# Kernel optimization log

Hardware: AMD Instinct MI355X
Metric: run time of the kernel (lower is better)

Reference implementation:

```python
import jax, jax.numpy as jnp
import numpy as np

MAX_WARPING_WINDOW = None  # matches init kwarg (None => full window, no masking)


def _pairwise_euclidean(x, y):
    # x: (B, F, Tx), y: (B, F, Ty) -> (B, Tx, Ty)
    # ||x_t - y_s||_2 computed via the expanded quadratic form (one GEMM instead
    # of materializing the (B, F, Tx, Ty) difference tensor like the torch code).
    x2 = jnp.sum(x * x, axis=1)                      # (B, Tx)
    y2 = jnp.sum(y * y, axis=1)                      # (B, Ty)
    xy = jnp.einsum('bft,bfs->bts', x, y)            # (B, Tx, Ty)
    d2 = jnp.maximum(x2[:, :, None] + y2[:, None, :] - 2.0 * xy, 0.0)
    return jnp.sqrt(d2)


def _dtw(cost):
    # cost: (B, Tx, Ty). Classic DTW DP:
    #   dtw[i, j] = cost[i-1, j-1] + min(dtw[i-1, j], dtw[i, j-1], dtw[i-1, j-1])
    # outer scan over rows i, inner scan over columns j (carries dtw[i, j-1]).
    B, Tx, Ty = cost.shape
    dt = cost.dtype
    INF = jnp.array(jnp.inf, dt)
    cost_t = jnp.transpose(cost, (1, 2, 0))          # (Tx, Ty, B)

    def row_step(carry, cost_row):
        prev_row, left = carry                       # prev_row: (Ty, B) = dtw[i-1, 1:], left: (B,) = dtw[i-1, 0]
        prev_shift = jnp.concatenate([left[None, :], prev_row[:-1]], axis=0)  # dtw[i-1, j-1]
        a = jnp.minimum(prev_row, prev_shift)        # min(dtw[i-1, j], dtw[i-1, j-1])

        def col_step(cur_left, ac):
            a_j, c_j = ac                            # each (B,)
            cur = c_j + jnp.minimum(a_j, cur_left)   # cur_left = dtw[i, j-1]
            return cur, cur

        _, cur_row = jax.lax.scan(col_step, jnp.full((B,), INF, dt), (a, cost_row))
        return (cur_row, jnp.full((B,), INF, dt)), None

    # row 0 of the DP: dtw[0, 0] = 0, dtw[0, j>0] = inf
    init = (jnp.full((Ty, B), INF, dt), jnp.zeros((B,), dt))
    (last_row, _), _ = jax.lax.scan(row_step, init, cost_t)
    return last_row[-1]                              # dtw[Tx, Ty], shape (B,)


def setup_inputs() -> dict:
    key = jax.random.key(0)
    kx, ky = jax.random.split(key)
    B, F, T = 128, 128, 512
    x = jax.random.normal(kx, (B, F, T), dtype=jnp.float32)
    y = jax.random.normal(ky, (B, F, T), dtype=jnp.float32)
    return {"x": x, "y": y}


def reference(x, y):
    cost = _pairwise_euclidean(x, y)                 # (B, Tx, Ty)
    if MAX_WARPING_WINDOW is not None:
        Tx, Ty = cost.shape[1], cost.shape[2]
        p = jnp.arange(Tx)[:, None]
        q = jnp.arange(Ty)[None, :]
        cost = jnp.where(jnp.abs(p - q) <= MAX_WARPING_WINDOW, cost, jnp.inf)
    return _dtw(cost)
```

## Files before the change

### kernel.cpp

```cpp
#include <hip/hip_runtime.h>
#include <stdint.h>

#define B_ 128
#define F_ 128
#define T_ 512
#define TS 64
#define DIAG_N 1024

#define BIGV 1e30f

typedef __attribute__((ext_vector_type(8))) short     bf16x8;
typedef __attribute__((ext_vector_type(4))) float     f32x4;
typedef __attribute__((ext_vector_type(8))) _Float16  half8;

static __device__ __forceinline__ unsigned short f32_to_bf16(float f) {
    union { float f; uint32_t u; } v; v.f = f;
    const uint32_t u = v.u + 0x7fffu + ((v.u >> 16) & 1u);
    return (unsigned short)(u >> 16);
}

static __device__ __forceinline__ float wave_shr1(float src, float fill) {
    const int r = __builtin_amdgcn_update_dpp(
        __builtin_bit_cast(int, fill), __builtin_bit_cast(int, src),
        0x138 , 0xf, 0xf, false);
    return __builtin_bit_cast(float, r);
}
static __device__ __forceinline__ float wave_shl1(float src, float fill) {
    const int r = __builtin_amdgcn_update_dpp(
        __builtin_bit_cast(int, fill), __builtin_bit_cast(int, src),
        0x130 , 0xf, 0xf, false);
    return __builtin_bit_cast(float, r);
}

__global__ __launch_bounds__(256) void dtw_prep_kernel(
    const float* __restrict__ x, const float* __restrict__ y,
    unsigned short* __restrict__ xt, unsigned short* __restrict__ yt,
    float* __restrict__ nx, float* __restrict__ ny)
{
    const int tch = blockIdx.x;
    const int b   = blockIdx.y;
    const int z   = blockIdx.z;
    const int tid = threadIdx.x;
    const int t0  = tch * 64;

    const float* src      = (z == 0 ? x : y) + (size_t)b * F_ * T_;
    unsigned short* dst   = (z == 0 ? xt : yt) + (size_t)b * T_ * F_;
    float* nd             = (z == 0 ? nx : ny) + (size_t)b * T_;

    __shared__ float S[F_][65];

    const int fr = tid >> 4;
    const int q  = (tid & 15) * 4;
#pragma unroll
    for (int p = 0; p < 8; ++p) {
        const int f = p * 16 + fr;
        const float4 v = *(const float4*)(src + (size_t)f * T_ + t0 + q);
        S[f][q] = v.x; S[f][q + 1] = v.y; S[f][q + 2] = v.z; S[f][q + 3] = v.w;
    }
    __syncthreads();

    if (tid < 64) {
        float s = 0.f;
#pragma unroll
        for (int f = 0; f < F_; ++f) { const float v = S[f][tid]; s = fmaf(v, v, s); }
        nd[t0 + tid] = s;
    }

    const int tl = tid >> 2;
    const int fb = (tid & 3) * 32;
    uint32_t pk[16];
#pragma unroll
    for (int e = 0; e < 16; ++e) {
        const uint32_t lo = f32_to_bf16(S[fb + 2 * e][tl]);
        const uint32_t hi = f32_to_bf16(S[fb + 2 * e + 1][tl]);
        pk[e] = lo | (hi << 16);
    }
    uint32_t* o = (uint32_t*)(dst + (size_t)(t0 + tl) * F_ + fb);
#pragma unroll
    for (int e = 0; e < 16; e += 4)
        *(uint4*)(o + e) = make_uint4(pk[e], pk[e + 1], pk[e + 2], pk[e + 3]);
}

__global__ __launch_bounds__(256) void dtw_cost_kernel(
    const unsigned short* __restrict__ xt, const unsigned short* __restrict__ yt,
    const float* __restrict__ nx, const float* __restrict__ ny,
    unsigned short* __restrict__ costD, int b0)
{
    const int tj  = blockIdx.x;
    const int ti  = blockIdx.y;
    const int bl  = blockIdx.z;
    const int b   = b0 + bl;
    const int tid = threadIdx.x;
    const int gi0 = ti * TS;
    const int gj0 = tj * TS;

    const int w    = tid >> 6;
    const int lane = tid & 63;
    const int l15  = lane & 15;
    const int hi   = lane >> 4;

    __shared__ __align__(16) char smem[16384];
    unsigned short* Ys = (unsigned short*)smem;

    {
        const int l16 = tid & 15;
#pragma unroll
        for (int p = 0; p < 4; ++p) {
            const int row = p * 16 + (tid >> 4);
            const uint4 vy = *(const uint4*)(yt + ((size_t)b * T_ + gj0 + row) * F_ + l16 * 8);
            const int byt = (row * 256 + l16 * 16) ^ ((row & 7) << 4);
            *(uint4*)((char*)Ys + byt) = vy;
        }
    }

    const unsigned short* xb = xt + ((size_t)b * T_ + gi0 + 16 * w + l15) * F_ + hi * 8;
    const bf16x8 A0 = *(const bf16x8*)(xb);
    const bf16x8 A1 = *(const bf16x8*)(xb + 32);
    const bf16x8 A2 = *(const bf16x8*)(xb + 64);
    const bf16x8 A3 = *(const bf16x8*)(xb + 96);

    const float4 x2r = *(const float4*)(nx + (size_t)b * T_ + gi0 + 16 * w + 4 * hi);
    float y2c[4];
#pragma unroll
    for (int nt = 0; nt < 4; ++nt)
        y2c[nt] = ny[(size_t)b * T_ + gj0 + nt * 16 + l15];
    const float x2v[4] = {x2r.x, x2r.y, x2r.z, x2r.w};

    __syncthreads();

    f32x4 acc[4] = {};
#pragma unroll
    for (int kb = 0; kb < 4; ++kb) {
        const int koff = kb * 64 + hi * 16;
        const bf16x8 a = (kb == 0) ? A0 : (kb == 1) ? A1 : (kb == 2) ? A2 : A3;
#pragma unroll
        for (int nt = 0; nt < 4; ++nt) {
            const int col = nt * 16 + l15;
            const bf16x8 bb = *(const bf16x8*)((const char*)Ys +
                               ((col * 256 + koff) ^ ((col & 7) << 4)));
            acc[nt] = __builtin_amdgcn_mfma_f32_16x16x32_bf16(a, bb, acc[nt], 0, 0, 0);
        }
    }

    __syncthreads();
    unsigned short* Ts = (unsigned short*)smem;
#pragma unroll
    for (int nt = 0; nt < 4; ++nt) {
        const int col = nt * 16 + l15;
#pragma unroll
        for (int r = 0; r < 4; ++r) {
            const int row = 16 * w + hi * 4 + r;
            const float c = sqrtf(fmaxf(x2v[r] + y2c[nt] - 2.f * acc[nt][r], 0.f));
            const _Float16 hv = (_Float16)c;
            Ts[row * 67 + col] = *(const unsigned short*)&hv;
        }
    }
    __syncthreads();

    unsigned short* outD = costD + (size_t)bl * (DIAG_N * (size_t)T_);
    const int tbase = gi0 + gj0;
#pragma unroll
    for (int q = 0; q < 16; ++q) {
        const int g = q * 4 + w;
        const int d = (lane <= g) ? g : g + 64;
        outD[(size_t)(tbase + d) * T_ + gj0 + lane] = Ts[(d - lane) * 67 + lane];
    }
}

__global__ __launch_bounds__(128, 1) void dtw_dp_bidi(
    const unsigned short* __restrict__ costD, float* __restrict__ out, int b0)
{
    const int bl  = blockIdx.x;
    const int tid = threadIdx.x;
    const int w   = tid >> 6;
    const int L   = tid & 63;
    const unsigned short* gbase = costD + (size_t)bl * (DIAG_N * (size_t)T_) + 8 * L;

    __shared__ __align__(16) unsigned short ringF[32][T_];
    __shared__ __align__(16) unsigned short ringB[32][T_];
    __shared__ __align__(16) float bb2[T_];
    __shared__ __align__(16) float bb3[T_];

    float va0 = BIGV, va1 = BIGV, va2 = BIGV, va3 = BIGV,
          va4 = BIGV, va5 = BIGV, va6 = BIGV, va7 = BIGV;
    float vb0 = BIGV, vb1 = BIGV, vb2 = BIGV, vb3 = BIGV,
          vb4 = BIGV, vb5 = BIGV, vb6 = BIGV, vb7 = BIGV;
    float s2c;
    half8 ca0, ca1, ca2, ca3, ca4, ca5, ca6, ca7;
    half8 cb0, cb1, cb2, cb3, cb4, cb5, cb6, cb7;

#define GLD(RING, row, slot)                                                \
    __builtin_amdgcn_global_load_lds(                                       \
        (const __attribute__((address_space(1))) void*)(gbase + (size_t)(row) * T_), \
        (__attribute__((address_space(3))) void*)(&RING[slot][0]), 16, 0, 0)

#define GLD8F(blk) do {                                                     \
    const int r0_ = (blk) * 8, s0_ = ((blk) & 3) * 8;                       \
    GLD(ringF, r0_ + 0, s0_ + 0); GLD(ringF, r0_ + 1, s0_ + 1);             \
    GLD(ringF, r0_ + 2, s0_ + 2); GLD(ringF, r0_ + 3, s0_ + 3);             \
    GLD(ringF, r0_ + 4, s0_ + 4); GLD(ringF, r0_ + 5, s0_ + 5);             \
    GLD(ringF, r0_ + 6, s0_ + 6); GLD(ringF, r0_ + 7, s0_ + 7);             \
} while (0)

#define GLD8B(blk) do {                                                     \
    const int v0_ = (blk) * 8, s0_ = ((blk) & 3) * 8;                       \
    GLD(ringB, 1022 - (v0_ + 0), s0_ + 0); GLD(ringB, 1022 - (v0_ + 1), s0_ + 1); \
    GLD(ringB, 1022 - (v0_ + 2), s0_ + 2); GLD(ringB, 1022 - (v0_ + 3), s0_ + 3); \
    GLD(ringB, 1022 - (v0_ + 4), s0_ + 4); GLD(ringB, 1022 - (v0_ + 5), s0_ + 5); \
    GLD(ringB, 1022 - (v0_ + 6), s0_ + 6); GLD(ringB, 1022 - (v0_ + 7), s0_ + 7); \
} while (0)

#define WAITV(n)                                                            \
    do { asm volatile("s_waitcnt vmcnt(" #n ")" ::: "memory");              \
         __builtin_amdgcn_sched_barrier(0); } while (0)

#define SB __builtin_amdgcn_sched_barrier(0)

#define RL8(RING, BK, blk) do {                                             \
    const unsigned short* rp_ = &RING[((blk) & 3) * 8][8 * L];              \
    BK##0 = *(const half8*)(rp_ + 0 * T_);                                  \
    BK##1 = *(const half8*)(rp_ + 1 * T_);                                  \
    BK##2 = *(const half8*)(rp_ + 2 * T_);                                  \
    BK##3 = *(const half8*)(rp_ + 3 * T_);                                  \
    BK##4 = *(const half8*)(rp_ + 4 * T_);                                  \
    BK##5 = *(const half8*)(rp_ + 5 * T_);                                  \
    BK##6 = *(const half8*)(rp_ + 6 * T_);                                  \
    BK##7 = *(const half8*)(rp_ + 7 * T_);                                  \
} while (0)

#define STEPF_A(hh) do {                                                    \
    const float s1 = wave_shr1(va7, BIGV);                                  \
    const float n0 = (float)hh[0] + fminf(fminf(va0, s1),  s2c);            \
    const float n1 = (float)hh[1] + fminf(fminf(va1, va0), vb0);            \
    const float n2 = (float)hh[2] + fminf(fminf(va2, va1), vb1);            \
    const float n3 = (float)hh[3] + fminf(fminf(va3, va2), vb2);            \
    const float n4 = (float)hh[4] + fminf(fminf(va4, va3), vb3);            \
    const float n5 = (float)hh[5] + fminf(fminf(va5, va4), vb4);            \
    const float n6 = (float)hh[6] + fminf(fminf(va6, va5), vb5);            \
    const float n7 = (float)hh[7] + fminf(fminf(va7, va6), vb6);            \
    s2c = s1;                                                               \
    vb0 = n0; vb1 = n1; vb2 = n2; vb3 = n3;                                 \
    vb4 = n4; vb5 = n5; vb6 = n6; vb7 = n7;                                 \
} while (0)

#define STEPF_B(hh) do {                                                    \
    const float s1 = wave_shr1(vb7, BIGV);                                  \
    const float n0 = (float)hh[0] + fminf(fminf(vb0, s1),  s2c);            \
    const float n1 = (float)hh[1] + fminf(fminf(vb1, vb0), va0);            \
    const float n2 = (float)hh[2] + fminf(fminf(vb2, vb1), va1);            \
    const float n3 = (float)hh[3] + fminf(fminf(vb3, vb2), va2);            \
    const float n4 = (float)hh[4] + fminf(fminf(vb4, vb3), va3);            \
    const float n5 = (float)hh[5] + fminf(fminf(vb5, vb4), va4);            \
    const float n6 = (float)hh[6] + fminf(fminf(vb6, vb5), va5);            \
    const float n7 = (float)hh[7] + fminf(fminf(vb7, vb6), va6);            \
    s2c = s1;                                                               \
    va0 = n0; va1 = n1; va2 = n2; va3 = n3;                                 \
    va4 = n4; va5 = n5; va6 = n6; va7 = n7;                                 \
} while (0)

#define STEPB_A(hh) do {                                                    \
    const float s1 = wave_shl1(va0, BIGV);                                  \
    const float n7 = (float)hh[7] + fminf(fminf(va7, s1),  s2c);            \
    const float n6 = (float)hh[6] + fminf(fminf(va6, va7), vb7);            \
    const float n5 = (float)hh[5] + fminf(fminf(va5, va6), vb6);            \
    const float n4 = (float)hh[4] + fminf(fminf(va4, va5), vb5);            \
    const float n3 = (float)hh[3] + fminf(fminf(va3, va4), vb4);            \
    const float n2 = (float)hh[2] + fminf(fminf(va2, va3), vb3);            \
    const float n1 = (float)hh[1] + fminf(fminf(va1, va2), vb2);            \
    const float n0 = (float)hh[0] + fminf(fminf(va0, va1), vb1);            \
    s2c = s1;                                                               \
    vb0 = n0; vb1 = n1; vb2 = n2; vb3 = n3;                                 \
    vb4 = n4; vb5 = n5; vb6 = n6; vb7 = n7;                                 \
} while (0)

#define STEPB_B(hh) do {                                                    \
    const float s1 = wave_shl1(vb0, BIGV);                                  \
    const float n7 = (float)hh[7] + fminf(fminf(vb7, s1),  s2c);            \
    const float n6 = (float)hh[6] + fminf(fminf(vb6, vb7), va7);            \
    const float n5 = (float)hh[5] + fminf(fminf(vb5, vb6), va6);            \
    const float n4 = (float)hh[4] + fminf(fminf(vb4, vb5), va5);            \
    const float n3 = (float)hh[3] + fminf(fminf(vb3, vb4), va4);            \
    const float n2 = (float)hh[2] + fminf(fminf(vb2, vb3), va3);            \
    const float n1 = (float)hh[1] + fminf(fminf(vb1, vb2), va2);            \
    const float n0 = (float)hh[0] + fminf(fminf(vb0, vb1), va1);            \
    s2c = s1;                                                               \
    va0 = n0; va1 = n1; va2 = n2; va3 = n3;                                 \
    va4 = n4; va5 = n5; va6 = n6; va7 = n7;                                 \
} while (0)

#define STEPF8(BK)                                                          \
    STEPF_A(BK##0); STEPF_B(BK##1); STEPF_A(BK##2); STEPF_B(BK##3);         \
    STEPF_A(BK##4); STEPF_B(BK##5); STEPF_A(BK##6); STEPF_B(BK##7)
#define STEPB8(BK)                                                          \
    STEPB_A(BK##0); STEPB_B(BK##1); STEPB_A(BK##2); STEPB_B(BK##3);         \
    STEPB_A(BK##4); STEPB_B(BK##5); STEPB_A(BK##6); STEPB_B(BK##7)

    if (w == 0) {
        s2c = (L == 0) ? 0.f : BIGV;
#pragma unroll
        for (int r = 0; r < 32; ++r) GLD(ringF, r, r);
        WAITV(24); RL8(ringF, ca, 0); SB;
        int k = 0;
#pragma unroll 1
        for (int it = 0; it < 30; ++it) {
            WAITV(16); RL8(ringF, cb, k + 1); SB; STEPF8(ca); SB; GLD8F(k + 4); SB;
            WAITV(16); RL8(ringF, ca, k + 2); SB; STEPF8(cb); SB; GLD8F(k + 5); SB;
            k += 2;
        }
        WAITV(16); RL8(ringF, cb, 61); SB; STEPF8(ca); SB;
        WAITV(8);  RL8(ringF, ca, 62); SB; STEPF8(cb); SB;
        WAITV(0);  RL8(ringF, cb, 63); SB; STEPF8(ca); SB;
        STEPF8(cb);
    } else {
        s2c = (L == 63) ? 0.f : BIGV;
#pragma unroll
        for (int r = 0; r < 32; ++r) GLD(ringB, 1022 - r, r);
        WAITV(24); RL8(ringB, ca, 0); SB;
        int k = 0;
#pragma unroll 1
        for (int it = 0; it < 30; ++it) {
            WAITV(16); RL8(ringB, cb, k + 1); SB; STEPB8(ca); SB; GLD8B(k + 4); SB;
            WAITV(16); RL8(ringB, ca, k + 2); SB; STEPB8(cb); SB; GLD8B(k + 5); SB;
            k += 2;
        }
        WAITV(16); RL8(ringB, cb, 61); SB; STEPB8(ca); SB;
        WAITV(8);  RL8(ringB, ca, 62); SB; STEPB8(cb); SB;
        WAITV(0);  RL8(ringB, cb, 63); SB; STEPB8(ca); SB;
        STEPB_A(cb0); STEPB_B(cb1); STEPB_A(cb2); STEPB_B(cb3);
        STEPB_A(cb4); STEPB_B(cb5); STEPB_A(cb6);
        *(float4*)&bb2[8 * L]     = make_float4(vb0, vb1, vb2, vb3);
        *(float4*)&bb2[8 * L + 4] = make_float4(vb4, vb5, vb6, vb7);
        *(float4*)&bb3[8 * L]     = make_float4(va0, va1, va2, va3);
        *(float4*)&bb3[8 * L + 4] = make_float4(va4, va5, va6, va7);
    }

    __syncthreads();

    if (w == 0) {
        const float4 p0 = *(const float4*)&bb2[8 * L];
        const float4 p1 = *(const float4*)&bb2[8 * L + 4];
        const float4 q0 = *(const float4*)&bb3[8 * L];
        const float4 q1 = *(const float4*)&bb3[8 * L + 4];
        const float b2[8] = {p0.x, p0.y, p0.z, p0.w, p1.x, p1.y, p1.z, p1.w};
        const float b3[8] = {q0.x, q0.y, q0.z, q0.w, q1.x, q1.y, q1.z, q1.w};
        const float F511[8] = {va0, va1, va2, va3, va4, va5, va6, va7};
        const float F510[8] = {vb0, vb1, vb2, vb3, vb4, vb5, vb6, vb7};
        float b2s[8], b3s[8];
#pragma unroll
        for (int kk = 0; kk < 7; ++kk) { b2s[kk] = b2[kk + 1]; b3s[kk] = b3[kk + 1]; }
        b2s[7] = wave_shl1(b2[0], BIGV);
        b3s[7] = wave_shl1(b3[0], BIGV);
        float m = BIGV;
#pragma unroll
        for (int kk = 0; kk < 8; ++kk) {
            const float t1 = F511[kk] + fminf(fminf(b2[kk], b2s[kk]), b3s[kk]);
            const float t2 = F510[kk] + b2s[kk];
            m = fminf(m, fminf(t1, t2));
        }
#pragma unroll
        for (int off = 1; off < 64; off <<= 1)
            m = fminf(m, __shfl_xor(m, off));
        if (L == 0) out[b0 + bl] = m;
    }

#undef GLD
#undef GLD8F
#undef GLD8B
#undef WAITV
#undef SB
#undef RL8
#undef STEPF_A
#undef STEPF_B
#undef STEPB_A
#undef STEPB_B
#undef STEPF8
#undef STEPB8
}

extern "C" void kernel_launch(void* const* d_in, const int* in_sizes, int n_in,
                              void* d_out, int out_size, void* d_ws, size_t ws_size,
                              hipStream_t stream)
{
    const float* x = (const float*)d_in[0];
    const float* y = (const float*)d_in[1];
    float* out = (float*)d_out;

    unsigned short* xt = (unsigned short*)d_ws;
    unsigned short* yt = xt + (size_t)B_ * T_ * F_;
    float* nx = (float*)(yt + (size_t)B_ * T_ * F_);
    float* ny = nx + (size_t)B_ * T_;
    unsigned short* costD = (unsigned short*)(ny + (size_t)B_ * T_);
    const size_t head = (size_t)((char*)costD - (char*)d_ws);

    const size_t perb = (size_t)DIAG_N * T_ * sizeof(unsigned short);
    int Bg = 8;
    for (int g = 128; g >= 8; g >>= 1)
        if (ws_size >= head + perb * (size_t)g) { Bg = g; break; }

    hipLaunchKernelGGL(dtw_prep_kernel, dim3(T_ / 64, B_, 2), dim3(256), 0, stream,
                       x, y, xt, yt, nx, ny);

    for (int b0 = 0; b0 < B_; b0 += Bg) {
        dim3 gc(T_ / TS, T_ / TS, Bg);
        hipLaunchKernelGGL(dtw_cost_kernel, gc, dim3(256), 0, stream,
                           xt, yt, nx, ny, costD, b0);
        hipLaunchKernelGGL(dtw_dp_bidi, dim3(Bg), dim3(128), 0, stream,
                           costD, out, b0);
    }
}
```

Baseline: 102.6 us.

## Fuse cost GEMM and DTW DP into one persistent kernel with per-band counters

Merges the tiled cost-matrix kernel and the bidirectional DP kernel into a single launch. The first 128 blocks run the DP, and the remaining blocks compute 64x64 cost tiles, issued in an order that alternates between the two ends of the anti-diagonal bands. Each DP wave waits on atomic per-band completion counters before streaming the next rows of diagonals, and the prefetch ring shrinks to three slots. The aim is to overlap cost generation with the serial DP and remove the batch-group launch loop, at the risk of spin-wait stalls and of deadlock if the DP blocks occupy CUs that producer blocks need.

Result: slower. 390.7 us (+280.7%).

```diff
diff --git a/kernel.cpp b/kernel.cpp
--- a/kernel.cpp
+++ b/kernel.cpp
@@ -4,8 +4,8 @@
 #define B_ 128
 #define F_ 128
 #define T_ 512
-#define TS 64
 #define DIAG_N 1024
+#define NDP 128
 
 #define BIGV 1e30f
 
@@ -22,20 +22,42 @@
 static __device__ __forceinline__ float wave_shr1(float src, float fill) {
     const int r = __builtin_amdgcn_update_dpp(
         __builtin_bit_cast(int, fill), __builtin_bit_cast(int, src),
-        0x138 , 0xf, 0xf, false);
+        0x138, 0xf, 0xf, false);
     return __builtin_bit_cast(float, r);
 }
 static __device__ __forceinline__ float wave_shl1(float src, float fill) {
     const int r = __builtin_amdgcn_update_dpp(
         __builtin_bit_cast(int, fill), __builtin_bit_cast(int, src),
-        0x130 , 0xf, 0xf, false);
+        0x130, 0xf, 0xf, false);
     return __builtin_bit_cast(float, r);
+}
+
+static __device__ __forceinline__ int band_need(int p) {
+    return 8 - (p > 7 ? p - 7 : 7 - p);
+}
+static __device__ __forceinline__ void gate_up(const int* cnt_b, int& done, int m) {
+    while (done < m) {
+        const int p = done + 1, need = band_need(p);
+        while (__hip_atomic_load(&cnt_b[p], __ATOMIC_ACQUIRE,
+                                 __HIP_MEMORY_SCOPE_AGENT) < need)
+            __builtin_amdgcn_s_sleep(2);
+        ++done;
+    }
+}
+static __device__ __forceinline__ void gate_down(const int* cnt_b, int& done, int m) {
+    while (done > m) {
+        const int p = done - 1, need = band_need(p);
+        while (__hip_atomic_load(&cnt_b[p], __ATOMIC_ACQUIRE,
+                                 __HIP_MEMORY_SCOPE_AGENT) < need)
+            __builtin_amdgcn_s_sleep(2);
+        --done;
+    }
 }
 
 __global__ __launch_bounds__(256) void dtw_prep_kernel(
     const float* __restrict__ x, const float* __restrict__ y,
     unsigned short* __restrict__ xt, unsigned short* __restrict__ yt,
-    float* __restrict__ nx, float* __restrict__ ny)
+    float* __restrict__ nx, float* __restrict__ ny, int* __restrict__ cnt)
 {
     const int tch = blockIdx.x;
     const int b   = blockIdx.y;
@@ -43,6 +65,8 @@
     const int tid = threadIdx.x;
     const int t0  = tch * 64;
 
+    if (tch == 0 && z == 0 && tid < 16) cnt[b * 16 + tid] = 0;
+
     const float* src      = (z == 0 ? x : y) + (size_t)b * F_ * T_;
     unsigned short* dst   = (z == 0 ? xt : yt) + (size_t)b * T_ * F_;
     float* nd             = (z == 0 ? nx : ny) + (size_t)b * T_;
@@ -81,133 +105,149 @@
         *(uint4*)(o + e) = make_uint4(pk[e], pk[e + 1], pk[e + 2], pk[e + 3]);
 }
 
-__global__ __launch_bounds__(256) void dtw_cost_kernel(
+__global__ __launch_bounds__(256, 1) void dtw_mega(
     const unsigned short* __restrict__ xt, const unsigned short* __restrict__ yt,
     const float* __restrict__ nx, const float* __restrict__ ny,
-    unsigned short* __restrict__ costD, int b0)
+    unsigned short* __restrict__ costD, int* __restrict__ cnt,
+    float* __restrict__ out)
 {
-    const int tj  = blockIdx.x;
-    const int ti  = blockIdx.y;
-    const int bl  = blockIdx.z;
-    const int b   = b0 + bl;
+    __shared__ __align__(16) char smem[53248];
     const int tid = threadIdx.x;
-    const int gi0 = ti * TS;
-    const int gj0 = tj * TS;
-
-    const int w    = tid >> 6;
-    const int lane = tid & 63;
-    const int l15  = lane & 15;
-    const int hi   = lane >> 4;
-
-    __shared__ __align__(16) char smem[16384];
-    unsigned short* Ys = (unsigned short*)smem;
-
-    {
-        const int l16 = tid & 15;
-#pragma unroll
-        for (int p = 0; p < 4; ++p) {
-            const int row = p * 16 + (tid >> 4);
-            const uint4 vy = *(const uint4*)(yt + ((size_t)b * T_ + gj0 + row) * F_ + l16 * 8);
-            const int byt = (row * 256 + l16 * 16) ^ ((row & 7) << 4);
-            *(uint4*)((char*)Ys + byt) = vy;
-        }
-    }
-
-    const unsigned short* xb = xt + ((size_t)b * T_ + gi0 + 16 * w + l15) * F_ + hi * 8;
-    const bf16x8 A0 = *(const bf16x8*)(xb);
-    const bf16x8 A1 = *(const bf16x8*)(xb + 32);
-    const bf16x8 A2 = *(const bf16x8*)(xb + 64);
-    const bf16x8 A3 = *(const bf16x8*)(xb + 96);
-
-    const float4 x2r = *(const float4*)(nx + (size_t)b * T_ + gi0 + 16 * w + 4 * hi);
-    float y2c[4];
-#pragma unroll
-    for (int nt = 0; nt < 4; ++nt)
-        y2c[nt] = ny[(size_t)b * T_ + gj0 + nt * 16 + l15];
-    const float x2v[4] = {x2r.x, x2r.y, x2r.z, x2r.w};
-
-    __syncthreads();
-
-    f32x4 acc[4] = {};
-#pragma unroll
-    for (int kb = 0; kb < 4; ++kb) {
-        const int koff = kb * 64 + hi * 16;
-        const bf16x8 a = (kb == 0) ? A0 : (kb == 1) ? A1 : (kb == 2) ? A2 : A3;
+
+    if (blockIdx.x >= NDP) {
+        const int g = blockIdx.x - NDP;
+        const int P[15] = {0,14,1,13,2,12,3,11,4,10,5,9,6,8,7};
+        int r = 0, base = 0, np = 1;
+        for (r = 0; r < 15; ++r) {
+            np = band_need(P[r]);
+            const int sz = np * B_;
+            if (g < base + sz) break;
+            base += sz;
+        }
+        const int rem = g - base;
+        const int bl  = rem & 127;
+        const int e   = rem >> 7;
+        const int p   = P[r];
+        const int ti  = (p > 7 ? p - 7 : 0) + e;
+        const int tj  = p - ti;
+        const int gi0 = ti * 64, gj0 = tj * 64;
+
+        const int w    = tid >> 6;
+        const int lane = tid & 63;
+        const int l15  = lane & 15;
+        const int hi   = lane >> 4;
+
+        unsigned short* Ys = (unsigned short*)smem;
+
+        {
+            const int l16 = tid & 15;
+#pragma unroll
+            for (int pp = 0; pp < 4; ++pp) {
+                const int row = pp * 16 + (tid >> 4);
+                const uint4 vy = *(const uint4*)(yt + ((size_t)bl * T_ + gj0 + row) * F_ + l16 * 8);
+                const int byt = (row * 256 + l16 * 16) ^ ((row & 7) << 4);
+                *(uint4*)((char*)Ys + byt) = vy;
+            }
+        }
+
+        const unsigned short* xb = xt + ((size_t)bl * T_ + gi0 + 16 * w + l15) * F_ + hi * 8;
+        const bf16x8 A0 = *(const bf16x8*)(xb);
+        const bf16x8 A1 = *(const bf16x8*)(xb + 32);
+        const bf16x8 A2 = *(const bf16x8*)(xb + 64);
+        const bf16x8 A3 = *(const bf16x8*)(xb + 96);
+
+        const float4 x2r = *(const float4*)(nx + (size_t)bl * T_ + gi0 + 16 * w + 4 * hi);
+        float y2c[4];
+#pragma unroll
+        for (int nt = 0; nt < 4; ++nt)
+            y2c[nt] = ny[(size_t)bl * T_ + gj0 + nt * 16 + l15];
+        const float x2v[4] = {x2r.x, x2r.y, x2r.z, x2r.w};
+
+        __syncthreads();
+
+        f32x4 acc[4] = {};
+#pragma unroll
+        for (int kb = 0; kb < 4; ++kb) {
+            const int koff = kb * 64 + hi * 16;
+            const bf16x8 a = (kb == 0) ? A0 : (kb == 1) ? A1 : (kb == 2) ? A2 : A3;
+#pragma unroll
+            for (int nt = 0; nt < 4; ++nt) {
+                const int col = nt * 16 + l15;
+                const bf16x8 bb = *(const bf16x8*)((const char*)Ys +
+                                   ((col * 256 + koff) ^ ((col & 7) << 4)));
+                acc[nt] = __builtin_amdgcn_mfma_f32_16x16x32_bf16(a, bb, acc[nt], 0, 0, 0);
+            }
+        }
+
+        __syncthreads();
+        unsigned short* Ts = (unsigned short*)smem;
 #pragma unroll
         for (int nt = 0; nt < 4; ++nt) {
             const int col = nt * 16 + l15;
-            const bf16x8 bb = *(const bf16x8*)((const char*)Ys +
-                               ((col * 256 + koff) ^ ((col & 7) << 4)));
-            acc[nt] = __builtin_amdgcn_mfma_f32_16x16x32_bf16(a, bb, acc[nt], 0, 0, 0);
-        }
-    }
-
-    __syncthreads();
-    unsigned short* Ts = (unsigned short*)smem;
-#pragma unroll
-    for (int nt = 0; nt < 4; ++nt) {
-        const int col = nt * 16 + l15;
-#pragma unroll
-        for (int r = 0; r < 4; ++r) {
-            const int row = 16 * w + hi * 4 + r;
-            const float c = sqrtf(fmaxf(x2v[r] + y2c[nt] - 2.f * acc[nt][r], 0.f));
-            const _Float16 hv = (_Float16)c;
-            Ts[row * 67 + col] = *(const unsigned short*)&hv;
-        }
-    }
-    __syncthreads();
-
-    unsigned short* outD = costD + (size_t)bl * (DIAG_N * (size_t)T_);
-    const int tbase = gi0 + gj0;
-#pragma unroll
-    for (int q = 0; q < 16; ++q) {
-        const int g = q * 4 + w;
-        const int d = (lane <= g) ? g : g + 64;
-        outD[(size_t)(tbase + d) * T_ + gj0 + lane] = Ts[(d - lane) * 67 + lane];
-    }
-}
-
-__global__ __launch_bounds__(128, 1) void dtw_dp_bidi(
-    const unsigned short* __restrict__ costD, float* __restrict__ out, int b0)
-{
-    const int bl  = blockIdx.x;
-    const int tid = threadIdx.x;
-    const int w   = tid >> 6;
-    const int L   = tid & 63;
+#pragma unroll
+            for (int rr = 0; rr < 4; ++rr) {
+                const int row = 16 * w + hi * 4 + rr;
+                const float c = sqrtf(fmaxf(x2v[rr] + y2c[nt] - 2.f * acc[nt][rr], 0.f));
+                const _Float16 hv = (_Float16)c;
+                Ts[row * 67 + col] = *(const unsigned short*)&hv;
+            }
+        }
+        __syncthreads();
+
+        unsigned short* outD = costD + (size_t)bl * (DIAG_N * (size_t)T_);
+        const int tbase = gi0 + gj0;
+#pragma unroll
+        for (int q = 0; q < 16; ++q) {
+            const int gg = q * 4 + w;
+            const int d  = (lane <= gg) ? gg : gg + 64;
+            outD[(size_t)(tbase + d) * T_ + gj0 + lane] = Ts[(d - lane) * 67 + lane];
+        }
+
+        __syncthreads();
+        if (tid == 0)
+            __hip_atomic_fetch_add(&cnt[bl * 16 + p], 1, __ATOMIC_RELEASE,
+                                   __HIP_MEMORY_SCOPE_AGENT);
+        return;
+    }
+
+    const int w  = tid >> 6;
+    const int L  = tid & 63;
+    const int bl = blockIdx.x;
     const unsigned short* gbase = costD + (size_t)bl * (DIAG_N * (size_t)T_) + 8 * L;
-
-    __shared__ __align__(16) unsigned short ringF[32][T_];
-    __shared__ __align__(16) unsigned short ringB[32][T_];
-    __shared__ __align__(16) float bb2[T_];
-    __shared__ __align__(16) float bb3[T_];
+    const int* cnt_b = cnt + bl * 16;
+
+    unsigned short (*ringF)[T_] = (unsigned short (*)[T_])(smem);
+    unsigned short (*ringB)[T_] = (unsigned short (*)[T_])(smem + 24576);
+    float* bb2 = (float*)(smem + 49152);
+    float* bb3 = (float*)(smem + 51200);
 
     float va0 = BIGV, va1 = BIGV, va2 = BIGV, va3 = BIGV,
           va4 = BIGV, va5 = BIGV, va6 = BIGV, va7 = BIGV;
     float vb0 = BIGV, vb1 = BIGV, vb2 = BIGV, vb3 = BIGV,
           vb4 = BIGV, vb5 = BIGV, vb6 = BIGV, vb7 = BIGV;
-    float s2c;
+    float s2c = BIGV;
     half8 ca0, ca1, ca2, ca3, ca4, ca5, ca6, ca7;
     half8 cb0, cb1, cb2, cb3, cb4, cb5, cb6, cb7;
 
-#define GLD(RING, row, slot)                                                \
+#define GLD(RING, row, slotrow)                                             \
     __builtin_amdgcn_global_load_lds(                                       \
         (const __attribute__((address_space(1))) void*)(gbase + (size_t)(row) * T_), \
-        (__attribute__((address_space(3))) void*)(&RING[slot][0]), 16, 0, 0)
-
-#define GLD8F(blk) do {                                                     \
-    const int r0_ = (blk) * 8, s0_ = ((blk) & 3) * 8;                       \
-    GLD(ringF, r0_ + 0, s0_ + 0); GLD(ringF, r0_ + 1, s0_ + 1);             \
-    GLD(ringF, r0_ + 2, s0_ + 2); GLD(ringF, r0_ + 3, s0_ + 3);             \
-    GLD(ringF, r0_ + 4, s0_ + 4); GLD(ringF, r0_ + 5, s0_ + 5);             \
-    GLD(ringF, r0_ + 6, s0_ + 6); GLD(ringF, r0_ + 7, s0_ + 7);             \
-} while (0)
-
-#define GLD8B(blk) do {                                                     \
-    const int v0_ = (blk) * 8, s0_ = ((blk) & 3) * 8;                       \
-    GLD(ringB, 1022 - (v0_ + 0), s0_ + 0); GLD(ringB, 1022 - (v0_ + 1), s0_ + 1); \
-    GLD(ringB, 1022 - (v0_ + 2), s0_ + 2); GLD(ringB, 1022 - (v0_ + 3), s0_ + 3); \
-    GLD(ringB, 1022 - (v0_ + 4), s0_ + 4); GLD(ringB, 1022 - (v0_ + 5), s0_ + 5); \
-    GLD(ringB, 1022 - (v0_ + 6), s0_ + 6); GLD(ringB, 1022 - (v0_ + 7), s0_ + 7); \
+        (__attribute__((address_space(3))) void*)(&RING[slotrow][0]), 16, 0, 0)
+
+#define GLD8F(blk, slot) do {                                               \
+    const int r0_ = (blk) * 8, q0_ = (slot) * 8;                            \
+    GLD(ringF, r0_ + 0, q0_ + 0); GLD(ringF, r0_ + 1, q0_ + 1);             \
+    GLD(ringF, r0_ + 2, q0_ + 2); GLD(ringF, r0_ + 3, q0_ + 3);             \
+    GLD(ringF, r0_ + 4, q0_ + 4); GLD(ringF, r0_ + 5, q0_ + 5);             \
+    GLD(ringF, r0_ + 6, q0_ + 6); GLD(ringF, r0_ + 7, q0_ + 7);             \
+} while (0)
+
+#define GLD8B(blk, slot) do {                                               \
+    const int v0_ = (blk) * 8, q0_ = (slot) * 8;                            \
+    GLD(ringB, 1022 - (v0_ + 0), q0_ + 0); GLD(ringB, 1022 - (v0_ + 1), q0_ + 1); \
+    GLD(ringB, 1022 - (v0_ + 2), q0_ + 2); GLD(ringB, 1022 - (v0_ + 3), q0_ + 3); \
+    GLD(ringB, 1022 - (v0_ + 4), q0_ + 4); GLD(ringB, 1022 - (v0_ + 5), q0_ + 5); \
+    GLD(ringB, 1022 - (v0_ + 6), q0_ + 6); GLD(ringB, 1022 - (v0_ + 7), q0_ + 7); \
 } while (0)
 
 #define WAITV(n)                                                            \
@@ -216,8 +256,8 @@
 
 #define SB __builtin_amdgcn_sched_barrier(0)
 
-#define RL8(RING, BK, blk) do {                                             \
-    const unsigned short* rp_ = &RING[((blk) & 3) * 8][8 * L];              \
+#define RL8S(RING, BK, slot) do {                                           \
+    const unsigned short* rp_ = &RING[(slot) * 8][8 * L];                   \
     BK##0 = *(const half8*)(rp_ + 0 * T_);                                  \
     BK##1 = *(const half8*)(rp_ + 1 * T_);                                  \
     BK##2 = *(const half8*)(rp_ + 2 * T_);                                  \
@@ -297,35 +337,51 @@
 
     if (w == 0) {
         s2c = (L == 0) ? 0.f : BIGV;
-#pragma unroll
-        for (int r = 0; r < 32; ++r) GLD(ringF, r, r);
-        WAITV(24); RL8(ringF, ca, 0); SB;
+        int fdone = -1;
+        gate_up(cnt_b, fdone, 0);
+        GLD8F(0, 0); GLD8F(1, 1);
+        WAITV(8); RL8S(ringF, ca, 0); SB;
+        GLD8F(2, 2);
         int k = 0;
 #pragma unroll 1
         for (int it = 0; it < 30; ++it) {
-            WAITV(16); RL8(ringF, cb, k + 1); SB; STEPF8(ca); SB; GLD8F(k + 4); SB;
-            WAITV(16); RL8(ringF, ca, k + 2); SB; STEPF8(cb); SB; GLD8F(k + 5); SB;
+            WAITV(8); RL8S(ringF, cb, (k + 1) % 3); SB;
+            if (((k + 3) & 7) == 0) gate_up(cnt_b, fdone, (k + 3) >> 3);
+            GLD8F(k + 3, k % 3); SB;
+            STEPF8(ca); SB;
+            WAITV(8); RL8S(ringF, ca, (k + 2) % 3); SB;
+            if (((k + 4) & 7) == 0) gate_up(cnt_b, fdone, (k + 4) >> 3);
+            GLD8F(k + 4, (k + 1) % 3); SB;
+            STEPF8(cb); SB;
             k += 2;
         }
-        WAITV(16); RL8(ringF, cb, 61); SB; STEPF8(ca); SB;
-        WAITV(8);  RL8(ringF, ca, 62); SB; STEPF8(cb); SB;
-        WAITV(0);  RL8(ringF, cb, 63); SB; STEPF8(ca); SB;
+        WAITV(8); RL8S(ringF, cb, 61 % 3); SB; GLD8F(63, 0); SB; STEPF8(ca); SB;
+        WAITV(8); RL8S(ringF, ca, 62 % 3); SB; STEPF8(cb); SB;
+        WAITV(0); RL8S(ringF, cb, 0);      SB; STEPF8(ca); SB;
         STEPF8(cb);
-    } else {
+    } else if (w == 1) {
         s2c = (L == 63) ? 0.f : BIGV;
-#pragma unroll
-        for (int r = 0; r < 32; ++r) GLD(ringB, 1022 - r, r);
-        WAITV(24); RL8(ringB, ca, 0); SB;
+        int bdone = 15;
+        gate_down(cnt_b, bdone, 14);
+        GLD8B(0, 0); GLD8B(1, 1);
+        WAITV(8); RL8S(ringB, ca, 0); SB;
+        GLD8B(2, 2);
         int k = 0;
 #pragma unroll 1
         for (int it = 0; it < 30; ++it) {
-            WAITV(16); RL8(ringB, cb, k + 1); SB; STEPB8(ca); SB; GLD8B(k + 4); SB;
-            WAITV(16); RL8(ringB, ca, k + 2); SB; STEPB8(cb); SB; GLD8B(k + 5); SB;
+            WAITV(8); RL8S(ringB, cb, (k + 1) % 3); SB;
+            if (((k + 3) & 7) == 0) gate_down(cnt_b, bdone, 14 - ((k + 3) >> 3));
+            GLD8B(k + 3, k % 3); SB;
+            STEPB8(ca); SB;
+            WAITV(8); RL8S(ringB, ca, (k + 2) % 3); SB;
+            if (((k + 4) & 7) == 0) gate_down(cnt_b, bdone, 14 - ((k + 4) >> 3));
+            GLD8B(k + 4, (k + 1) % 3); SB;
+            STEPB8(cb); SB;
             k += 2;
         }
-        WAITV(16); RL8(ringB, cb, 61); SB; STEPB8(ca); SB;
-        WAITV(8);  RL8(ringB, ca, 62); SB; STEPB8(cb); SB;
-        WAITV(0);  RL8(ringB, cb, 63); SB; STEPB8(ca); SB;
+        WAITV(8); RL8S(ringB, cb, 61 % 3); SB; GLD8B(63, 0); SB; STEPB8(ca); SB;
+        WAITV(8); RL8S(ringB, ca, 62 % 3); SB; STEPB8(cb); SB;
+        WAITV(0); RL8S(ringB, cb, 0);      SB; STEPB8(ca); SB;
         STEPB_A(cb0); STEPB_B(cb1); STEPB_A(cb2); STEPB_B(cb3);
         STEPB_A(cb4); STEPB_B(cb5); STEPB_A(cb6);
         *(float4*)&bb2[8 * L]     = make_float4(vb0, vb1, vb2, vb3);
@@ -333,7 +389,6 @@
         *(float4*)&bb3[8 * L]     = make_float4(va0, va1, va2, va3);
         *(float4*)&bb3[8 * L + 4] = make_float4(va4, va5, va6, va7);
     }
-
     __syncthreads();
 
     if (w == 0) {
@@ -360,7 +415,7 @@
 #pragma unroll
         for (int off = 1; off < 64; off <<= 1)
             m = fminf(m, __shfl_xor(m, off));
-        if (L == 0) out[b0 + bl] = m;
+        if (L == 0) out[bl] = m;
     }
 
 #undef GLD
@@ -368,7 +423,7 @@
 #undef GLD8B
 #undef WAITV
 #undef SB
-#undef RL8
+#undef RL8S
 #undef STEPF_A
 #undef STEPF_B
 #undef STEPB_A
@@ -390,21 +445,10 @@
     float* nx = (float*)(yt + (size_t)B_ * T_ * F_);
     float* ny = nx + (size_t)B_ * T_;
     unsigned short* costD = (unsigned short*)(ny + (size_t)B_ * T_);
-    const size_t head = (size_t)((char*)costD - (char*)d_ws);
-
-    const size_t perb = (size_t)DIAG_N * T_ * sizeof(unsigned short);
-    int Bg = 8;
-    for (int g = 128; g >= 8; g >>= 1)
-        if (ws_size >= head + perb * (size_t)g) { Bg = g; break; }
+    int* cnt = (int*)(costD + (size_t)B_ * DIAG_N * T_);
 
     hipLaunchKernelGGL(dtw_prep_kernel, dim3(T_ / 64, B_, 2), dim3(256), 0, stream,
-                       x, y, xt, yt, nx, ny);
-
-    for (int b0 = 0; b0 < B_; b0 += Bg) {
-        dim3 gc(T_ / TS, T_ / TS, Bg);
-        hipLaunchKernelGGL(dtw_cost_kernel, gc, dim3(256), 0, stream,
-                           xt, yt, nx, ny, costD, b0);
-        hipLaunchKernelGGL(dtw_dp_bidi, dim3(Bg), dim3(128), 0, stream,
-                           costD, out, b0);
-    }
-}
+                       x, y, xt, yt, nx, ny, cnt);
+    hipLaunchKernelGGL(dtw_mega, dim3(NDP + 64 * B_), dim3(256), 0, stream,
+                       xt, yt, nx, ny, costD, cnt, out);
+}
```

## Store diagonal cost matrix in FP8 to halve DP kernel traffic

Applied to the files above, without the earlier changes.

The cost kernel now converts each fp16 cost to FP8 before writing the diagonal-major buffer. The DP kernel streams FP8 rows with 16-byte loads that each cover two diagonal rows, so it issues half as many global-to-LDS loads. It unpacks the values with packed fp8-to-f32 conversions and reverses the row order for the backward pass. This halves intermediate memory traffic and workspace per batch, which may allow larger batch groups. The cost is much coarser cost values that accumulate through the DP sum, a real accuracy risk.

After: 97.03 us (median of 2 runs). -5.4%, faster.

```diff
diff --git a/kernel.cpp b/kernel.cpp
--- a/kernel.cpp
+++ b/kernel.cpp
@@ -11,7 +11,7 @@
 
 typedef __attribute__((ext_vector_type(8))) short     bf16x8;
 typedef __attribute__((ext_vector_type(4))) float     f32x4;
-typedef __attribute__((ext_vector_type(8))) _Float16  half8;
+typedef __attribute__((ext_vector_type(2))) float     f32x2;
 
 static __device__ __forceinline__ unsigned short f32_to_bf16(float f) {
     union { float f; uint32_t u; } v; v.f = f;
@@ -22,13 +22,13 @@
 static __device__ __forceinline__ float wave_shr1(float src, float fill) {
     const int r = __builtin_amdgcn_update_dpp(
         __builtin_bit_cast(int, fill), __builtin_bit_cast(int, src),
-        0x138 , 0xf, 0xf, false);
+        0x138, 0xf, 0xf, false);
     return __builtin_bit_cast(float, r);
 }
 static __device__ __forceinline__ float wave_shl1(float src, float fill) {
     const int r = __builtin_amdgcn_update_dpp(
         __builtin_bit_cast(int, fill), __builtin_bit_cast(int, src),
-        0x130 , 0xf, 0xf, false);
+        0x130, 0xf, 0xf, false);
     return __builtin_bit_cast(float, r);
 }
 
@@ -84,7 +84,7 @@
 __global__ __launch_bounds__(256) void dtw_cost_kernel(
     const unsigned short* __restrict__ xt, const unsigned short* __restrict__ yt,
     const float* __restrict__ nx, const float* __restrict__ ny,
-    unsigned short* __restrict__ costD, int b0)
+    unsigned char* __restrict__ costD, int b0)
 {
     const int tj  = blockIdx.x;
     const int ti  = blockIdx.y;
@@ -157,27 +157,30 @@
     }
     __syncthreads();
 
-    unsigned short* outD = costD + (size_t)bl * (DIAG_N * (size_t)T_);
+    unsigned char* outD = costD + (size_t)bl * (DIAG_N * (size_t)T_);
     const int tbase = gi0 + gj0;
 #pragma unroll
     for (int q = 0; q < 16; ++q) {
         const int g = q * 4 + w;
         const int d = (lane <= g) ? g : g + 64;
-        outD[(size_t)(tbase + d) * T_ + gj0 + lane] = Ts[(d - lane) * 67 + lane];
+        const _Float16 hval = *(const _Float16*)&Ts[(d - lane) * 67 + lane];
+        const float cf = (float)hval;
+        const int pk = __builtin_amdgcn_cvt_pk_fp8_f32(cf, cf, 0, false);
+        outD[(size_t)(tbase + d) * T_ + gj0 + lane] = (unsigned char)pk;
     }
 }
 
 __global__ __launch_bounds__(128, 1) void dtw_dp_bidi(
-    const unsigned short* __restrict__ costD, float* __restrict__ out, int b0)
+    const unsigned char* __restrict__ costD, float* __restrict__ out, int b0)
 {
     const int bl  = blockIdx.x;
     const int tid = threadIdx.x;
     const int w   = tid >> 6;
     const int L   = tid & 63;
-    const unsigned short* gbase = costD + (size_t)bl * (DIAG_N * (size_t)T_) + 8 * L;
-
-    __shared__ __align__(16) unsigned short ringF[32][T_];
-    __shared__ __align__(16) unsigned short ringB[32][T_];
+    const unsigned char* gbase = costD + (size_t)bl * (DIAG_N * (size_t)T_) + 16 * L;
+
+    __shared__ __align__(16) unsigned char ringF[32][T_];
+    __shared__ __align__(16) unsigned char ringB[32][T_];
     __shared__ __align__(16) float bb2[T_];
     __shared__ __align__(16) float bb3[T_];
 
@@ -186,28 +189,24 @@
     float vb0 = BIGV, vb1 = BIGV, vb2 = BIGV, vb3 = BIGV,
           vb4 = BIGV, vb5 = BIGV, vb6 = BIGV, vb7 = BIGV;
     float s2c;
-    half8 ca0, ca1, ca2, ca3, ca4, ca5, ca6, ca7;
-    half8 cb0, cb1, cb2, cb3, cb4, cb5, cb6, cb7;
-
-#define GLD(RING, row, slot)                                                \
+    uint2 ca0, ca1, ca2, ca3, ca4, ca5, ca6, ca7;
+    uint2 cb0, cb1, cb2, cb3, cb4, cb5, cb6, cb7;
+
+#define GLDP(RING, row, slot)                                               \
     __builtin_amdgcn_global_load_lds(                                       \
         (const __attribute__((address_space(1))) void*)(gbase + (size_t)(row) * T_), \
         (__attribute__((address_space(3))) void*)(&RING[slot][0]), 16, 0, 0)
 
-#define GLD8F(blk) do {                                                     \
+#define GLD4F(blk) do {                                                     \
     const int r0_ = (blk) * 8, s0_ = ((blk) & 3) * 8;                       \
-    GLD(ringF, r0_ + 0, s0_ + 0); GLD(ringF, r0_ + 1, s0_ + 1);             \
-    GLD(ringF, r0_ + 2, s0_ + 2); GLD(ringF, r0_ + 3, s0_ + 3);             \
-    GLD(ringF, r0_ + 4, s0_ + 4); GLD(ringF, r0_ + 5, s0_ + 5);             \
-    GLD(ringF, r0_ + 6, s0_ + 6); GLD(ringF, r0_ + 7, s0_ + 7);             \
-} while (0)
-
-#define GLD8B(blk) do {                                                     \
-    const int v0_ = (blk) * 8, s0_ = ((blk) & 3) * 8;                       \
-    GLD(ringB, 1022 - (v0_ + 0), s0_ + 0); GLD(ringB, 1022 - (v0_ + 1), s0_ + 1); \
-    GLD(ringB, 1022 - (v0_ + 2), s0_ + 2); GLD(ringB, 1022 - (v0_ + 3), s0_ + 3); \
-    GLD(ringB, 1022 - (v0_ + 4), s0_ + 4); GLD(ringB, 1022 - (v0_ + 5), s0_ + 5); \
-    GLD(ringB, 1022 - (v0_ + 6), s0_ + 6); GLD(ringB, 1022 - (v0_ + 7), s0_ + 7); \
+    GLDP(ringF, r0_ + 0, s0_ + 0); GLDP(ringF, r0_ + 2, s0_ + 2);           \
+    GLDP(ringF, r0_ + 4, s0_ + 4); GLDP(ringF, r0_ + 6, s0_ + 6);           \
+} while (0)
+
+#define GLD4B(blk) do {                                                     \
+    const int m0_ = 1015 - (blk) * 8, s0_ = ((blk) & 3) * 8;                \
+    GLDP(ringB, m0_ + 0, s0_ + 0); GLDP(ringB, m0_ + 2, s0_ + 2);           \
+    GLDP(ringB, m0_ + 4, s0_ + 4); GLDP(ringB, m0_ + 6, s0_ + 6);           \
 } while (0)
 
 #define WAITV(n)                                                            \
@@ -216,73 +215,95 @@
 
 #define SB __builtin_amdgcn_sched_barrier(0)
 
-#define RL8(RING, BK, blk) do {                                             \
-    const unsigned short* rp_ = &RING[((blk) & 3) * 8][8 * L];              \
-    BK##0 = *(const half8*)(rp_ + 0 * T_);                                  \
-    BK##1 = *(const half8*)(rp_ + 1 * T_);                                  \
-    BK##2 = *(const half8*)(rp_ + 2 * T_);                                  \
-    BK##3 = *(const half8*)(rp_ + 3 * T_);                                  \
-    BK##4 = *(const half8*)(rp_ + 4 * T_);                                  \
-    BK##5 = *(const half8*)(rp_ + 5 * T_);                                  \
-    BK##6 = *(const half8*)(rp_ + 6 * T_);                                  \
-    BK##7 = *(const half8*)(rp_ + 7 * T_);                                  \
-} while (0)
-
-#define STEPF_A(hh) do {                                                    \
+#define RL8(BK, blk) do {                                                   \
+    const unsigned char* rp_ = &ringF[((blk) & 3) * 8][8 * L];              \
+    BK##0 = *(const uint2*)(rp_ + 0 * T_);                                  \
+    BK##1 = *(const uint2*)(rp_ + 1 * T_);                                  \
+    BK##2 = *(const uint2*)(rp_ + 2 * T_);                                  \
+    BK##3 = *(const uint2*)(rp_ + 3 * T_);                                  \
+    BK##4 = *(const uint2*)(rp_ + 4 * T_);                                  \
+    BK##5 = *(const uint2*)(rp_ + 5 * T_);                                  \
+    BK##6 = *(const uint2*)(rp_ + 6 * T_);                                  \
+    BK##7 = *(const uint2*)(rp_ + 7 * T_);                                  \
+} while (0)
+
+#define RL8R(BK, blk) do {                                                  \
+    const unsigned char* rp_ = &ringB[((blk) & 3) * 8][8 * L];              \
+    BK##0 = *(const uint2*)(rp_ + 7 * T_);                                  \
+    BK##1 = *(const uint2*)(rp_ + 6 * T_);                                  \
+    BK##2 = *(const uint2*)(rp_ + 5 * T_);                                  \
+    BK##3 = *(const uint2*)(rp_ + 4 * T_);                                  \
+    BK##4 = *(const uint2*)(rp_ + 3 * T_);                                  \
+    BK##5 = *(const uint2*)(rp_ + 2 * T_);                                  \
+    BK##6 = *(const uint2*)(rp_ + 1 * T_);                                  \
+    BK##7 = *(const uint2*)(rp_ + 0 * T_);                                  \
+} while (0)
+
+#define CVT8(Hv)                                                            \
+    const f32x2 c01 = __builtin_amdgcn_cvt_pk_f32_fp8((int)Hv.x, false);    \
+    const f32x2 c23 = __builtin_amdgcn_cvt_pk_f32_fp8((int)Hv.x, true);     \
+    const f32x2 c45 = __builtin_amdgcn_cvt_pk_f32_fp8((int)Hv.y, false);    \
+    const f32x2 c67 = __builtin_amdgcn_cvt_pk_f32_fp8((int)Hv.y, true)
+
+#define STEPF_A(Hv) do {                                                    \
     const float s1 = wave_shr1(va7, BIGV);                                  \
-    const float n0 = (float)hh[0] + fminf(fminf(va0, s1),  s2c);            \
-    const float n1 = (float)hh[1] + fminf(fminf(va1, va0), vb0);            \
-    const float n2 = (float)hh[2] + fminf(fminf(va2, va1), vb1);            \
-    const float n3 = (float)hh[3] + fminf(fminf(va3, va2), vb2);            \
-    const float n4 = (float)hh[4] + fminf(fminf(va4, va3), vb3);            \
-    const float n5 = (float)hh[5] + fminf(fminf(va5, va4), vb4);            \
-    const float n6 = (float)hh[6] + fminf(fminf(va6, va5), vb5);            \
-    const float n7 = (float)hh[7] + fminf(fminf(va7, va6), vb6);            \
+    CVT8(Hv);                                                               \
+    const float n0 = c01[0] + fminf(fminf(va0, s1),  s2c);                  \
+    const float n1 = c01[1] + fminf(fminf(va1, va0), vb0);                  \
+    const float n2 = c23[0] + fminf(fminf(va2, va1), vb1);                  \
+    const float n3 = c23[1] + fminf(fminf(va3, va2), vb2);                  \
+    const float n4 = c45[0] + fminf(fminf(va4, va3), vb3);                  \
+    const float n5 = c45[1] + fminf(fminf(va5, va4), vb4);                  \
+    const float n6 = c67[0] + fminf(fminf(va6, va5), vb5);                  \
+    const float n7 = c67[1] + fminf(fminf(va7, va6), vb6);                  \
     s2c = s1;                                                               \
     vb0 = n0; vb1 = n1; vb2 = n2; vb3 = n3;                                 \
     vb4 = n4; vb5 = n5; vb6 = n6; vb7 = n7;                                 \
 } while (0)
 
-#define STEPF_B(hh) do {                                                    \
+#define STEPF_B(Hv) do {                                                    \
     const float s1 = wave_shr1(vb7, BIGV);                                  \
-    const float n0 = (float)hh[0] + fminf(fminf(vb0, s1),  s2c);            \
-    const float n1 = (float)hh[1] + fminf(fminf(vb1, vb0), va0);            \
-    const float n2 = (float)hh[2] + fminf(fminf(vb2, vb1), va1);            \
-    const float n3 = (float)hh[3] + fminf(fminf(vb3, vb2), va2);            \
-    const float n4 = (float)hh[4] + fminf(fminf(vb4, vb3), va3);            \
-    const float n5 = (float)hh[5] + fminf(fminf(vb5, vb4), va4);            \
-    const float n6 = (float)hh[6] + fminf(fminf(vb6, vb5), va5);            \
-    const float n7 = (float)hh[7] + fminf(fminf(vb7, vb6), va6);            \
+    CVT8(Hv);                                                               \
+    const float n0 = c01[0] + fminf(fminf(vb0, s1),  s2c);                  \
+    const float n1 = c01[1] + fminf(fminf(vb1, vb0), va0);                  \
+    const float n2 = c23[0] + fminf(fminf(vb2, vb1), va1);                  \
+    const float n3 = c23[1] + fminf(fminf(vb3, vb2), va2);                  \
+    const float n4 = c45[0] + fminf(fminf(vb4, vb3), va3);                  \
+    const float n5 = c45[1] + fminf(fminf(vb5, vb4), va4);                  \
+    const float n6 = c67[0] + fminf(fminf(vb6, vb5), va5);                  \
+    const float n7 = c67[1] + fminf(fminf(vb7, vb6), va6);                  \
     s2c = s1;                                                               \
     va0 = n0; va1 = n1; va2 = n2; va3 = n3;                                 \
     va4 = n4; va5 = n5; va6 = n6; va7 = n7;                                 \
 } while (0)
 
-#define STEPB_A(hh) do {                                                    \
+#define STEPB_A(Hv) do {                                                    \
     const float s1 = wave_shl1(va0, BIGV);                                  \
-    const float n7 = (float)hh[7] + fminf(fminf(va7, s1),  s2c);            \
-    const float n6 = (float)hh[6] + fminf(fminf(va6, va7), vb7);            \
-    const float n5 = (float)hh[5] + fminf(fminf(va5, va6), vb6);            \
-    const float n4 = (float)hh[4] + fminf(fminf(va4, va5), vb5);            \
-    const float n3 = (float)hh[3] + fminf(fminf(va3, va4), vb4);            \
-    const float n2 = (float)hh[2] + fminf(fminf(va2, va3), vb3);            \
-    const float n1 = (float)hh[1] + fminf(fminf(va1, va2), vb2);            \
-    const float n0 = (float)hh[0] + fminf(fminf(va0, va1), vb1);            \
+    CVT8(Hv);                                                               \
+    const float n7 = c67[1] + fminf(fminf(va7, s1),  s2c);                  \
+    const float n6 = c67[0] + fminf(fminf(va6, va7), vb7);                  \
+    const float n5 = c45[1] + fminf(fminf(va5, va6), vb6);                  \
+    const float n4 = c45[0] + fminf(fminf(va4, va5), vb5);                  \
+    const float n3 = c23[1] + fminf(fminf(va3, va4), vb4);                  \
+    const float n2 = c23[0] + fminf(fminf(va2, va3), vb3);                  \
+    const float n1 = c01[1] + fminf(fminf(va1, va2), vb2);                  \
+    const float n0 = c01[0] + fminf(fminf(va0, va1), vb1);                  \
     s2c = s1;                                                               \
     vb0 = n0; vb1 = n1; vb2 = n2; vb3 = n3;                                 \
     vb4 = n4; vb5 = n5; vb6 = n6; vb7 = n7;                                 \
 } while (0)
 
-#define STEPB_B(hh) do {                                                    \
+#define STEPB_B(Hv) do {                                                    \
     const float s1 = wave_shl1(vb0, BIGV);                                  \
-    const float n7 = (float)hh[7] + fminf(fminf(vb7, s1),  s2c);            \
-    const float n6 = (float)hh[6] + fminf(fminf(vb6, vb7), va7);            \
-    const float n5 = (float)hh[5] + fminf(fminf(vb5, vb6), va6);            \
-    const float n4 = (float)hh[4] + fminf(fminf(vb4, vb5), va5);            \
-    const float n3 = (float)hh[3] + fminf(fminf(vb3, vb4), va4);            \
-    const float n2 = (float)hh[2] + fminf(fminf(vb2, vb3), va3);            \
-    const float n1 = (float)hh[1] + fminf(fminf(vb1, vb2), va2);            \
-    const float n0 = (float)hh[0] + fminf(fminf(vb0, vb1), va1);            \
+    CVT8(Hv);                                                               \
+    const float n7 = c67[1] + fminf(fminf(vb7, s1),  s2c);                  \
+    const float n6 = c67[0] + fminf(fminf(vb6, vb7), va7);                  \
+    const float n5 = c45[1] + fminf(fminf(vb5, vb6), va6);                  \
+    const float n4 = c45[0] + fminf(fminf(vb4, vb5), va5);                  \
+    const float n3 = c23[1] + fminf(fminf(vb3, vb4), va4);                  \
+    const float n2 = c23[0] + fminf(fminf(vb2, vb3), va3);                  \
+    const float n1 = c01[1] + fminf(fminf(vb1, vb2), va2);                  \
+    const float n0 = c01[0] + fminf(fminf(vb0, vb1), va1);                  \
     s2c = s1;                                                               \
     va0 = n0; va1 = n1; va2 = n2; va3 = n3;                                 \
     va4 = n4; va5 = n5; va6 = n6; va7 = n7;                                 \
@@ -297,35 +318,33 @@
 
     if (w == 0) {
         s2c = (L == 0) ? 0.f : BIGV;
-#pragma unroll
-        for (int r = 0; r < 32; ++r) GLD(ringF, r, r);
-        WAITV(24); RL8(ringF, ca, 0); SB;
+        GLD4F(0); GLD4F(1); GLD4F(2); GLD4F(3);
+        WAITV(12); RL8(ca, 0); SB;
         int k = 0;
 #pragma unroll 1
         for (int it = 0; it < 30; ++it) {
-            WAITV(16); RL8(ringF, cb, k + 1); SB; STEPF8(ca); SB; GLD8F(k + 4); SB;
-            WAITV(16); RL8(ringF, ca, k + 2); SB; STEPF8(cb); SB; GLD8F(k + 5); SB;
+            WAITV(8); RL8(cb, k + 1); SB; STEPF8(ca); SB; GLD4F(k + 4); SB;
+            WAITV(8); RL8(ca, k + 2); SB; STEPF8(cb); SB; GLD4F(k + 5); SB;
             k += 2;
         }
-        WAITV(16); RL8(ringF, cb, 61); SB; STEPF8(ca); SB;
-        WAITV(8);  RL8(ringF, ca, 62); SB; STEPF8(cb); SB;
-        WAITV(0);  RL8(ringF, cb, 63); SB; STEPF8(ca); SB;
+        WAITV(8); RL8(cb, 61); SB; STEPF8(ca); SB;
+        WAITV(4); RL8(ca, 62); SB; STEPF8(cb); SB;
+        WAITV(0); RL8(cb, 63); SB; STEPF8(ca); SB;
         STEPF8(cb);
     } else {
         s2c = (L == 63) ? 0.f : BIGV;
-#pragma unroll
-        for (int r = 0; r < 32; ++r) GLD(ringB, 1022 - r, r);
-        WAITV(24); RL8(ringB, ca, 0); SB;
+        GLD4B(0); GLD4B(1); GLD4B(2); GLD4B(3);
+        WAITV(12); RL8R(ca, 0); SB;
         int k = 0;
 #pragma unroll 1
         for (int it = 0; it < 30; ++it) {
-            WAITV(16); RL8(ringB, cb, k + 1); SB; STEPB8(ca); SB; GLD8B(k + 4); SB;
-            WAITV(16); RL8(ringB, ca, k + 2); SB; STEPB8(cb); SB; GLD8B(k + 5); SB;
+            WAITV(8); RL8R(cb, k + 1); SB; STEPB8(ca); SB; GLD4B(k + 4); SB;
+            WAITV(8); RL8R(ca, k + 2); SB; STEPB8(cb); SB; GLD4B(k + 5); SB;
             k += 2;
         }
-        WAITV(16); RL8(ringB, cb, 61); SB; STEPB8(ca); SB;
-        WAITV(8);  RL8(ringB, ca, 62); SB; STEPB8(cb); SB;
-        WAITV(0);  RL8(ringB, cb, 63); SB; STEPB8(ca); SB;
+        WAITV(8); RL8R(cb, 61); SB; STEPB8(ca); SB;
+        WAITV(4); RL8R(ca, 62); SB; STEPB8(cb); SB;
+        WAITV(0); RL8R(cb, 63); SB; STEPB8(ca); SB;
         STEPB_A(cb0); STEPB_B(cb1); STEPB_A(cb2); STEPB_B(cb3);
         STEPB_A(cb4); STEPB_B(cb5); STEPB_A(cb6);
         *(float4*)&bb2[8 * L]     = make_float4(vb0, vb1, vb2, vb3);
@@ -363,12 +382,14 @@
         if (L == 0) out[b0 + bl] = m;
     }
 
-#undef GLD
-#undef GLD8F
-#undef GLD8B
+#undef GLDP
+#undef GLD4F
+#undef GLD4B
 #undef WAITV
 #undef SB
 #undef RL8
+#undef RL8R
+#undef CVT8
 #undef STEPF_A
 #undef STEPF_B
 #undef STEPB_A
@@ -389,10 +410,10 @@
     unsigned short* yt = xt + (size_t)B_ * T_ * F_;
     float* nx = (float*)(yt + (size_t)B_ * T_ * F_);
     float* ny = nx + (size_t)B_ * T_;
-    unsigned short* costD = (unsigned short*)(ny + (size_t)B_ * T_);
-    const size_t head = (size_t)((char*)costD - (char*)d_ws);
-
-    const size_t perb = (size_t)DIAG_N * T_ * sizeof(unsigned short);
+    unsigned char* costD = (unsigned char*)(ny + (size_t)B_ * T_);
+    const size_t head = (size_t)(costD - (unsigned char*)d_ws);
+
+    const size_t perb = (size_t)DIAG_N * T_;
     int Bg = 8;
     for (int g = 128; g >= 8; g >>= 1)
         if (ws_size >= head + perb * (size_t)g) { Bg = g; break; }
```
